# Performance work log

Hardware: AMD Instinct MI355X
Metric: run time of the kernel (lower is better)

## Reference

```python
import math
import jax, jax.numpy as jnp
import numpy as np

B, S, DIM, H = 16, 1024, 1024, 16
HD = DIM // H            # head_dim = 64
ROPE_DIM = HD // 2       # 32; per-axis rotary dim
FT = 32                  # ft_seq_len, FT*FT == S
PT = 16                  # pt_seq_len
THETA = 10000.0
EPS = 1e-6


def _rope_cos_sin():
    # freqs_for='lang'
    freqs = 1.0 / THETA ** (jnp.arange(0, ROPE_DIM, 2, dtype=jnp.float32) / ROPE_DIM)  # [ROPE_DIM//2]
    t = jnp.arange(FT, dtype=jnp.float32) / FT * PT                                    # [FT]
    fs = jnp.einsum('n,f->nf', t, freqs)                                               # [FT, ROPE_DIM//2]
    fs = jnp.repeat(fs, 2, axis=-1)                                                    # [FT, ROPE_DIM]
    fh = jnp.broadcast_to(fs[:, None, :], (FT, FT, ROPE_DIM))
    fw = jnp.broadcast_to(fs[None, :, :], (FT, FT, ROPE_DIM))
    f = jnp.concatenate([fh, fw], axis=-1).reshape(-1, 2 * ROPE_DIM)                   # [S, HD]
    return jnp.cos(f), jnp.sin(f)


def _rotate_half(x):
    x1, x2 = jnp.split(x, 2, axis=-1)
    return jnp.concatenate((-x2, x1), axis=-1)


def _rms_norm(x, w):
    xf = x.astype(jnp.float32)
    var = jnp.mean(jnp.square(xf), axis=-1, keepdims=True)
    return (w * (xf * jax.lax.rsqrt(var + EPS))).astype(x.dtype)


def setup_inputs() -> dict:
    key = jax.random.key(0)
    ks = jax.random.split(key, 4)
    sd = 1.0 / math.sqrt(DIM)
    return {
        'x': jax.random.normal(ks[0], (B, S, DIM), dtype=jnp.float32),
        'w_qkv': jax.random.normal(ks[1], (DIM, 3 * DIM), dtype=jnp.float32) * sd,
        'b_qkv': jnp.zeros((3 * DIM,), dtype=jnp.float32),
        'q_norm_w': jnp.ones((HD,), dtype=jnp.float32),
        'k_norm_w': jnp.ones((HD,), dtype=jnp.float32),
        'w_out': jax.random.normal(ks[2], (DIM, DIM), dtype=jnp.float32) * sd,
        'b_out': jnp.zeros((DIM,), dtype=jnp.float32),
    }


def reference(x, w_qkv, b_qkv, q_norm_w, k_norm_w, w_out, b_out):
    cos, sin = _rope_cos_sin()                    # [S, HD] each
    cos = cos[None, None].astype(x.dtype)
    sin = sin[None, None].astype(x.dtype)

    qkv = x @ w_qkv + b_qkv                       # [B,S,3*DIM]
    qkv = qkv.reshape(B, S, 3, H, HD).transpose(2, 0, 3, 1, 4)  # [3,B,H,S,HD]
    q, k, v = qkv[0], qkv[1], qkv[2]

    q = _rms_norm(q, q_norm_w)
    k = _rms_norm(k, k_norm_w)

    q = q * cos + _rotate_half(q) * sin
    k = k * cos + _rotate_half(k) * sin

    scale = 1.0 / math.sqrt(HD)
    logits = jnp.einsum('bhqd,bhkd->bhqk', q.astype(jnp.float32), k.astype(jnp.float32)) * scale
    attn = jax.nn.softmax(logits, axis=-1).astype(x.dtype)
    out = jnp.einsum('bhqk,bhkd->bhqd', attn, v)  # [B,H,S,HD]

    out = out.transpose(0, 2, 1, 3).reshape(B, S, DIM)
    return out @ w_out + b_out
```

## Files before the change

kernel.cpp:

```cpp
#include <hip/hip_runtime.h>
#include <cstdint>
#include <cstddef>

#define B_    16
#define S_    1024
#define DIM_  1024
#define H_    16
#define HD_   64
#define TDIM  3072

typedef unsigned short ushort_t;
typedef unsigned int   uint_t;
typedef __attribute__((ext_vector_type(8))) short s8v;
typedef __attribute__((ext_vector_type(4))) float f32x4;

__device__ __forceinline__ float b2f(ushort_t u) {
    union { uint_t i; float f; } t; t.i = (uint_t)u << 16; return t.f;
}
__device__ __forceinline__ ushort_t f2b(float f) {
    union { float f; uint_t i; } t; t.f = f;
    uint_t r = t.i + 0x7FFFu + ((t.i >> 16) & 1u);
    return (ushort_t)(r >> 16);
}

__device__ __forceinline__ f32x4 mfma_bf16(s8v a, s8v b, f32x4 c) {
    asm volatile("v_mfma_f32_16x16x32_bf16 %0, %1, %2, %0" : "+v"(c) : "v"(a), "v"(b));
    return c;
}

__device__ __forceinline__ void gload16(const void* g, void* l) {
    __builtin_amdgcn_global_load_lds(
        (const __attribute__((address_space(1))) uint_t*)g,
        (__attribute__((address_space(3))) uint_t*)l, 16, 0, 0);
}

__global__ __launch_bounds__(256) void f32_to_bf16_vec(const float* __restrict__ src,
                                                       short* __restrict__ dst, int n8) {
    int i = blockIdx.x * 256 + threadIdx.x;
    if (i < n8) {
        float4 a = *(const float4*)(src + (size_t)i * 8);
        float4 b = *(const float4*)(src + (size_t)i * 8 + 4);
        s8v t;
        t[0] = (short)f2b(a.x); t[1] = (short)f2b(a.y);
        t[2] = (short)f2b(a.z); t[3] = (short)f2b(a.w);
        t[4] = (short)f2b(b.x); t[5] = (short)f2b(b.y);
        t[6] = (short)f2b(b.z); t[7] = (short)f2b(b.w);
        *(s8v*)(dst + (size_t)i * 8) = t;
    }
}

__global__ __launch_bounds__(256) void rope_tables(float* __restrict__ cos_t,
                                                   float* __restrict__ sin_t) {
    int idx = blockIdx.x * 256 + threadIdx.x;
    int s = idx >> 6;
    int d = idx & 63;
    int pos = (d < 32) ? (s >> 5) : (s & 31);
    int i   = (d & 31) >> 1;
    float freq  = expf(-(float)i * 0.5756462732485115f);
    float angle = (float)pos * 0.5f * freq;
    cos_t[idx] = cosf(angle);
    sin_t[idx] = sinf(angle);
}

__global__ __launch_bounds__(256) void transpose_to_bf16(const float* __restrict__ Wsrc,
                                                         short* __restrict__ WT,
                                                         int K, int N) {
    __shared__ float t[32][33];
    int tx = threadIdx.x & 31, ty = threadIdx.x >> 5;
    int n0 = blockIdx.x * 32, k0 = blockIdx.y * 32;
#pragma unroll
    for (int i = 0; i < 4; ++i)
        t[ty + 8 * i][tx] = Wsrc[(size_t)(k0 + ty + 8 * i) * N + n0 + tx];
    __syncthreads();
#pragma unroll
    for (int i = 0; i < 4; ++i)
        WT[(size_t)(n0 + ty + 8 * i) * K + k0 + tx] = (short)f2b(t[tx][ty + 8 * i]);
}

template<typename CT, bool NORM>
__global__ __launch_bounds__(256) void gemm_glds(
        const short* __restrict__ A, const short* __restrict__ BT,
        const float* __restrict__ bias, CT* __restrict__ C,
        int M, int N, int K, int NX,
        const float* __restrict__ qw, const float* __restrict__ kw,
        const float* __restrict__ cos_t, const float* __restrict__ sin_t) {
    __shared__ short As[128 * 64];
    __shared__ short Bs[128 * 64];

    const int tid  = threadIdx.x;
    const int w    = tid >> 6;
    const int lane = tid & 63;
    const int l15  = lane & 15, lg = lane >> 4;

    const int nwg  = gridDim.x;
    const int cpx  = nwg >> 3;
    const int wgid = (blockIdx.x & 7) * cpx + (blockIdx.x >> 3);
    const int bx = wgid % NX, by = wgid / NX;
    const int m0 = by * 128, n0 = bx * 128;
    const int wr = (w >> 1) * 64, wc = (w & 1) * 64;

    const int srow = w * 32 + (lane >> 3);
    const int sk   = (lane & 7) * 8;

    f32x4 acc[4][4] = {};

    for (int k0 = 0; k0 < K; k0 += 64) {
        __syncthreads();
#pragma unroll
        for (int i = 0; i < 4; ++i) {
            int r = srow + i * 8;
            gload16(A  + (size_t)(m0 + r) * K + k0 + sk, &As[(w * 4 + i) * 512]);
            gload16(BT + (size_t)(n0 + r) * K + k0 + sk, &Bs[(w * 4 + i) * 512]);
        }
        __syncthreads();

#pragma unroll
        for (int kk = 0; kk < 2; ++kk) {
            s8v af[4], bf[4];
#pragma unroll
            for (int i = 0; i < 4; ++i) {
                af[i] = *(const s8v*)&As[(wr + 16 * i + l15) * 64 + kk * 32 + lg * 8];
                bf[i] = *(const s8v*)&Bs[(wc + 16 * i + l15) * 64 + kk * 32 + lg * 8];
            }
#pragma unroll
            for (int mi = 0; mi < 4; ++mi)
#pragma unroll
                for (int ni = 0; ni < 4; ++ni)
                    acc[mi][ni] = mfma_bf16(af[mi], bf[ni], acc[mi][ni]);
        }
    }

    if constexpr (NORM) {
        if (n0 + wc < 2048) {
            const float* nw = (n0 + wc < 1024) ? qw : kw;
            float wv[4], bv[4];
#pragma unroll
            for (int ni = 0; ni < 4; ++ni) {
                wv[ni] = nw[16 * ni + l15];
                bv[ni] = bias[n0 + wc + 16 * ni + l15];
            }
#pragma unroll
            for (int mi = 0; mi < 4; ++mi) {
#pragma unroll
                for (int r = 0; r < 4; ++r) {
                    int row = m0 + wr + 16 * mi + lg * 4 + r;
                    int s = row & (S_ - 1);
                    float v[4];
#pragma unroll
                    for (int ni = 0; ni < 4; ++ni) v[ni] = acc[mi][ni][r] + bv[ni];
                    float ss = v[0]*v[0] + v[1]*v[1] + v[2]*v[2] + v[3]*v[3];
                    ss += __shfl_xor(ss, 1);
                    ss += __shfl_xor(ss, 2);
                    ss += __shfl_xor(ss, 4);
                    ss += __shfl_xor(ss, 8);
                    float rms = rsqrtf(ss * (1.0f / 64.0f) + 1e-6f);
                    float xn[4];
#pragma unroll
                    for (int ni = 0; ni < 4; ++ni) xn[ni] = v[ni] * rms * wv[ni];
#pragma unroll
                    for (int ni = 0; ni < 4; ++ni) {
                        int d = 16 * ni + l15;
                        float c  = cos_t[s * 64 + d];
                        float sn = sin_t[s * 64 + d];
                        float rot = (ni < 2) ? -xn[ni + 2] : xn[ni - 2];
                        C[(size_t)row * N + n0 + wc + d] = (short)f2b(xn[ni] * c + rot * sn);
                    }
                }
            }
            return;
        }
    }
#pragma unroll
    for (int ni = 0; ni < 4; ++ni) {
        float bvv = bias[n0 + wc + 16 * ni + l15];
#pragma unroll
        for (int mi = 0; mi < 4; ++mi) {
#pragma unroll
            for (int r = 0; r < 4; ++r) {
                size_t row = (size_t)(m0 + wr + 16 * mi + lg * 4 + r);
                int    col = n0 + wc + 16 * ni + l15;
                float v = acc[mi][ni][r] + bvv;
                if constexpr (sizeof(CT) == 4) C[row * N + col] = v;
                else                           C[row * N + col] = (short)f2b(v);
            }
        }
    }
}

__global__ __launch_bounds__(256) void attn_mfma(const short* __restrict__ qkv,
                                                 short* __restrict__ attn) {
    __shared__ ushort_t Ks[64][72];
    __shared__ ushort_t Vt[64][72];
    __shared__ ushort_t Ps[4][32][72];

    const int tid  = threadIdx.x;
    const int w    = tid >> 6;
    const int lane = tid & 63;
    const int l15  = lane & 15, lg = lane >> 4;
    const int bh = blockIdx.y, b = bh >> 4, h = bh & 15;
    const int q0 = blockIdx.x * 128;

    const short* qbase = qkv + (size_t)b * S_ * TDIM + h * HD_;
    const short* kb = qbase + DIM_;
    const short* vb = qbase + 2 * DIM_;

    s8v qf[2][2];
#pragma unroll
    for (int mq = 0; mq < 2; ++mq)
#pragma unroll
        for (int kk = 0; kk < 2; ++kk)
            qf[mq][kk] = *(const s8v*)(qbase + (size_t)(q0 + w * 32 + mq * 16 + l15) * TDIM
                                       + kk * 32 + lg * 8);

    f32x4 of[2][4] = {};
    float m_s[2] = {-1e30f, -1e30f};
    float l_s[2] = {0.f, 0.f};

    const int kr   = tid >> 3;
    const int kp8  = (tid & 7) * 8;
    const int vkp  = tid >> 3;
    const int va   = tid & 7;
    const int vp8  = va * 8;
    const int vcol = (2 * vkp) ^ ((va & 3) << 4);

    s8v kA, kB, vA, vB;
    auto prefetch = [&](int kt) {
        const short* kbt = kb + (size_t)kt * 64 * TDIM;
        const short* vbt = vb + (size_t)kt * 64 * TDIM;
        kA = *(const s8v*)(kbt + (size_t)kr * TDIM + kp8);
        kB = *(const s8v*)(kbt + (size_t)(kr + 32) * TDIM + kp8);
        vA = *(const s8v*)(vbt + (size_t)(2 * vkp) * TDIM + vp8);
        vB = *(const s8v*)(vbt + (size_t)(2 * vkp + 1) * TDIM + vp8);
    };
    prefetch(0);

    for (int kt = 0; kt < 16; ++kt) {
        *(s8v*)&Ks[kr][kp8]      = kA;
        *(s8v*)&Ks[kr + 32][kp8] = kB;
#pragma unroll
        for (int j = 0; j < 8; ++j) {
            uint_t pk = (ushort_t)vA[j] | ((uint_t)(ushort_t)vB[j] << 16);
            *(uint_t*)&Vt[vp8 + j][vcol] = pk;
        }
        __syncthreads();

        if (kt < 15) prefetch(kt + 1);

        f32x4 st[4][2] = {};
#pragma unroll
        for (int kk = 0; kk < 2; ++kk) {
            s8v kf[4];
#pragma unroll
            for (int nk = 0; nk < 4; ++nk)
                kf[nk] = *(const s8v*)&Ks[nk * 16 + l15][kk * 32 + lg * 8];
#pragma unroll
            for (int nk = 0; nk < 4; ++nk)
#pragma unroll
                for (int mq = 0; mq < 2; ++mq)
                    st[nk][mq] = mfma_bf16(kf[nk], qf[mq][kk], st[nk][mq]);
        }

#pragma unroll
        for (int mq = 0; mq < 2; ++mq) {
            float mx = -1e30f;
#pragma unroll
            for (int nk = 0; nk < 4; ++nk)
#pragma unroll
                for (int r = 0; r < 4; ++r) {
                    st[nk][mq][r] *= 0.125f;
                    mx = fmaxf(mx, st[nk][mq][r]);
                }
            mx = fmaxf(mx, __shfl_xor(mx, 16));
            mx = fmaxf(mx, __shfl_xor(mx, 32));
            float mnew  = fmaxf(m_s[mq], mx);
            float alpha = __expf(m_s[mq] - mnew);
            m_s[mq] = mnew;

            float ls = 0.f;
#pragma unroll
            for (int nk = 0; nk < 4; ++nk) {
#pragma unroll
                for (int r = 0; r < 4; ++r) {
                    float p = __expf(st[nk][mq][r] - mnew);
                    st[nk][mq][r] = p;
                    ls += p;
                }
            }
            ls += __shfl_xor(ls, 16);
            ls += __shfl_xor(ls, 32);
            l_s[mq] = l_s[mq] * alpha + ls;

#pragma unroll
            for (int nk = 0; nk < 4; ++nk) {
                ushort4 pk;
                pk.x = f2b(st[nk][mq][0]); pk.y = f2b(st[nk][mq][1]);
                pk.z = f2b(st[nk][mq][2]); pk.w = f2b(st[nk][mq][3]);
                *(ushort4*)&Ps[w][mq * 16 + l15][nk * 16 + lg * 4] = pk;
            }

            float a4[4];
#pragma unroll
            for (int r = 0; r < 4; ++r) a4[r] = __shfl(alpha, lg * 4 + r);
#pragma unroll
            for (int nd = 0; nd < 4; ++nd)
#pragma unroll
                for (int r = 0; r < 4; ++r) of[mq][nd][r] *= a4[r];
        }

#pragma unroll
        for (int kk = 0; kk < 2; ++kk) {
            s8v pf[2], vf[4];
#pragma unroll
            for (int mq = 0; mq < 2; ++mq)
                pf[mq] = *(const s8v*)&Ps[w][mq * 16 + l15][kk * 32 + lg * 8];
#pragma unroll
            for (int nd = 0; nd < 4; ++nd) {
                int swz = (2 * nd + (l15 >> 3)) & 3;
                vf[nd] = *(const s8v*)&Vt[nd * 16 + l15][(kk * 32 + lg * 8) ^ (swz << 4)];
            }
#pragma unroll
            for (int mq = 0; mq < 2; ++mq)
#pragma unroll
                for (int nd = 0; nd < 4; ++nd)
                    of[mq][nd] = mfma_bf16(pf[mq], vf[nd], of[mq][nd]);
        }
        __syncthreads();
    }

#pragma unroll
    for (int mq = 0; mq < 2; ++mq) {
        float rinv = 1.0f / l_s[mq];
        float iv[4];
#pragma unroll
        for (int r = 0; r < 4; ++r) iv[r] = __shfl(rinv, lg * 4 + r);
#pragma unroll
        for (int nd = 0; nd < 4; ++nd)
#pragma unroll
            for (int r = 0; r < 4; ++r) {
                int row = q0 + w * 32 + mq * 16 + lg * 4 + r;
                attn[((size_t)b * S_ + row) * DIM_ + h * HD_ + nd * 16 + l15] =
                    (short)f2b(of[mq][nd][r] * iv[r]);
            }
    }
}

extern "C" void kernel_launch(void* const* d_in, const int* in_sizes, int n_in,
                              void* d_out, int out_size, void* d_ws, size_t ws_size,
                              hipStream_t stream) {
    const float* x        = (const float*)d_in[0];
    const float* w_qkv    = (const float*)d_in[1];
    const float* b_qkv    = (const float*)d_in[2];
    const float* q_norm_w = (const float*)d_in[3];
    const float* k_norm_w = (const float*)d_in[4];
    const float* w_out    = (const float*)d_in[5];
    const float* b_out    = (const float*)d_in[6];
    float* out = (float*)d_out;

    const size_t OFF_QKV = 0;
    const size_t OFF_ATT = 100663296;
    const size_t OFF_XB  = OFF_ATT + 33554432;
    const size_t OFF_WQ  = OFF_XB + 33554432;
    const size_t OFF_WO  = OFF_WQ + 6291456;
    const size_t OFF_CT  = OFF_WO + 2097152;
    const size_t OFF_ST  = OFF_CT + 262144;
    const size_t NEED    = OFF_ST + 262144;

    if (ws_size < NEED) {
        hipMemsetAsync(d_out, 0, (size_t)out_size * sizeof(float), stream);
        return;
    }

    char* ws = (char*)d_ws;
    short* qkv   = (short*)(ws + OFF_QKV);
    short* attnb = (short*)(ws + OFF_ATT);
    short* xb    = (short*)(ws + OFF_XB);
    short* wqkvT = (short*)(ws + OFF_WQ);
    short* woutT = (short*)(ws + OFF_WO);
    float* cos_t = (float*)(ws + OFF_CT);
    float* sin_t = (float*)(ws + OFF_ST);

    rope_tables<<<dim3(256), dim3(256), 0, stream>>>(cos_t, sin_t);
    f32_to_bf16_vec<<<dim3(8192), dim3(256), 0, stream>>>(x, xb, 2097152);
    transpose_to_bf16<<<dim3(96, 32), dim3(256), 0, stream>>>(w_qkv, wqkvT, 1024, 3072);
    transpose_to_bf16<<<dim3(32, 32), dim3(256), 0, stream>>>(w_out, woutT, 1024, 1024);

    gemm_glds<short, true><<<dim3(3072), dim3(256), 0, stream>>>(
        xb, wqkvT, b_qkv, qkv, 16384, 3072, 1024, 24,
        q_norm_w, k_norm_w, cos_t, sin_t);

    attn_mfma<<<dim3(8, 256), dim3(256), 0, stream>>>(qkv, attnb);

    gemm_glds<float, false><<<dim3(1024), dim3(256), 0, stream>>>(
        attnb, woutT, b_out, out, 16384, 1024, 1024, 8,
        nullptr, nullptr, nullptr, nullptr);
}
```

Before: 346.1 us.

## Use exp2 softmax with lazy rescaling, packed bf16 convert and MFMA priority

Folds the 1/sqrt(d) scale and log2(e) into one FMA feeding exp2, and skips the running-max rescale of the output accumulator unless the new max exceeds the old by a threshold, wave-uniformly. It also replaces manual bf16 rounding with the hardware packed convert, and raises wave priority around MFMA blocks. The aim is to cut VALU work in the online softmax. The lazy rescale lets probabilities grow up to 2^11 before renormalising, which is accurate in fp32 but lets unnormalised values feed bf16 P.

```diff
diff --git a/kernel.cpp b/kernel.cpp
--- a/kernel.cpp
+++ b/kernel.cpp
@@ -21,6 +21,11 @@
     union { float f; uint_t i; } t; t.f = f;
     uint_t r = t.i + 0x7FFFu + ((t.i >> 16) & 1u);
     return (ushort_t)(r >> 16);
+}
+__device__ __forceinline__ uint_t cvt_pk_bf16(float a, float b) {
+    uint_t r;
+    asm("v_cvt_pk_bf16_f32 %0, %1, %2" : "=v"(r) : "v"(a), "v"(b));
+    return r;
 }
 
 __device__ __forceinline__ f32x4 mfma_bf16(s8v a, s8v b, f32x4 c) {
@@ -193,6 +198,9 @@
     __shared__ ushort_t Vt[64][72];
     __shared__ ushort_t Ps[4][32][72];
 
+    const float SC  = 0.18033688011112042f;
+    const float THR = 11.0f;
+
     const int tid  = threadIdx.x;
     const int w    = tid >> 6;
     const int lane = tid & 63;
@@ -247,6 +255,7 @@
         if (kt < 15) prefetch(kt + 1);
 
         f32x4 st[4][2] = {};
+        __builtin_amdgcn_s_setprio(1);
 #pragma unroll
         for (int kk = 0; kk < 2; ++kk) {
             s8v kf[4];
@@ -259,6 +268,7 @@
                 for (int mq = 0; mq < 2; ++mq)
                     st[nk][mq] = mfma_bf16(kf[nk], qf[mq][kk], st[nk][mq]);
         }
+        __builtin_amdgcn_s_setprio(0);
 
 #pragma unroll
         for (int mq = 0; mq < 2; ++mq) {
@@ -266,47 +276,51 @@
 #pragma unroll
             for (int nk = 0; nk < 4; ++nk)
 #pragma unroll
-                for (int r = 0; r < 4; ++r) {
-                    st[nk][mq][r] *= 0.125f;
+                for (int r = 0; r < 4; ++r)
                     mx = fmaxf(mx, st[nk][mq][r]);
-                }
             mx = fmaxf(mx, __shfl_xor(mx, 16));
             mx = fmaxf(mx, __shfl_xor(mx, 32));
-            float mnew  = fmaxf(m_s[mq], mx);
-            float alpha = __expf(m_s[mq] - mnew);
-            m_s[mq] = mnew;
-
+            float mxs = mx * SC;
+
+            if (!__all(mxs <= m_s[mq] + THR)) {
+                float mnew  = fmaxf(m_s[mq], mxs);
+                float alpha = exp2f(m_s[mq] - mnew);
+                m_s[mq] = mnew;
+                l_s[mq] *= alpha;
+                float a4[4];
+#pragma unroll
+                for (int r = 0; r < 4; ++r) a4[r] = __shfl(alpha, lg * 4 + r);
+#pragma unroll
+                for (int nd = 0; nd < 4; ++nd)
+#pragma unroll
+                    for (int r = 0; r < 4; ++r) of[mq][nd][r] *= a4[r];
+            }
+
+            float m = m_s[mq];
             float ls = 0.f;
 #pragma unroll
             for (int nk = 0; nk < 4; ++nk) {
 #pragma unroll
                 for (int r = 0; r < 4; ++r) {
-                    float p = __expf(st[nk][mq][r] - mnew);
+                    float p = exp2f(__builtin_fmaf(st[nk][mq][r], SC, -m));
                     st[nk][mq][r] = p;
                     ls += p;
                 }
             }
             ls += __shfl_xor(ls, 16);
             ls += __shfl_xor(ls, 32);
-            l_s[mq] = l_s[mq] * alpha + ls;
+            l_s[mq] += ls;
 
 #pragma unroll
             for (int nk = 0; nk < 4; ++nk) {
-                ushort4 pk;
-                pk.x = f2b(st[nk][mq][0]); pk.y = f2b(st[nk][mq][1]);
-                pk.z = f2b(st[nk][mq][2]); pk.w = f2b(st[nk][mq][3]);
-                *(ushort4*)&Ps[w][mq * 16 + l15][nk * 16 + lg * 4] = pk;
-            }
-
-            float a4[4];
-#pragma unroll
-            for (int r = 0; r < 4; ++r) a4[r] = __shfl(alpha, lg * 4 + r);
-#pragma unroll
-            for (int nd = 0; nd < 4; ++nd)
-#pragma unroll
-                for (int r = 0; r < 4; ++r) of[mq][nd][r] *= a4[r];
-        }
-
+                uint2 pk2;
+                pk2.x = cvt_pk_bf16(st[nk][mq][0], st[nk][mq][1]);
+                pk2.y = cvt_pk_bf16(st[nk][mq][2], st[nk][mq][3]);
+                *(uint2*)&Ps[w][mq * 16 + l15][nk * 16 + lg * 4] = pk2;
+            }
+        }
+
+        __builtin_amdgcn_s_setprio(1);
 #pragma unroll
         for (int kk = 0; kk < 2; ++kk) {
             s8v pf[2], vf[4];
@@ -324,6 +338,7 @@
                 for (int nd = 0; nd < 4; ++nd)
                     of[mq][nd] = mfma_bf16(pf[mq], vf[nd], of[mq][nd]);
         }
+        __builtin_amdgcn_s_setprio(0);
         __syncthreads();
     }
 
```

Result: no change. 346.1 us (-0.0%).
